# Kernel tuning notes

Hardware: AMD Instinct MI355X
Metric: run time of the kernel (lower is better)

## Reference

```python
import jax, jax.numpy as jnp
import numpy as np

TEMPERATURE = 0.4
N, D = 8192, 128

def _l2norm(x):
    return x / jnp.maximum(jnp.linalg.norm(x, axis=-1, keepdims=True), 1e-12)

def _semi_loss(z1, z2, temp):
    z1n = _l2norm(z1)
    z2n = _l2norm(z2)
    refl = jnp.exp(jnp.matmul(z1n, z1n.T) / temp)      # [N, N]
    between = jnp.exp(jnp.matmul(z1n, z2n.T) / temp)   # [N, N]
    pos = jnp.diagonal(between)
    denom = refl.sum(axis=1) + between.sum(axis=1) - jnp.diagonal(refl)
    return -jnp.log(pos / denom)

def setup_inputs() -> dict:
    key = jax.random.key(0)
    k1, k2 = jax.random.split(key)
    out = jax.random.normal(k1, (N, D), dtype=jnp.float32)
    aug_out = jax.random.normal(k2, (N, D), dtype=jnp.float32)
    return {"out": out, "aug_out": aug_out}

def reference(out, aug_out):
    l1 = _semi_loss(out, aug_out, TEMPERATURE)
    l2 = _semi_loss(aug_out, out, TEMPERATURE)
    loss = (l1 + l2) * 0.5
    return loss.mean()
```

## Files before the change

kernel.cpp:

```cpp
#include <hip/hip_runtime.h>
#include <hip/hip_bf16.h>

#define NR  8192
#define M   16384
#define SUBB 16384

constexpr float INV_T   = 2.5f;
constexpr float SCALE_S = 1.89914134f;
constexpr float E_REFL  = 12.182493960703473f;
constexpr unsigned UNIT_E8M0 = 0x7F7F7F7Fu;

typedef int   i32x4 __attribute__((ext_vector_type(4)));
typedef int   i32x8 __attribute__((ext_vector_type(8)));
typedef float f32x4 __attribute__((ext_vector_type(4)));

typedef const __attribute__((address_space(1))) unsigned int* gas_u32;
typedef __attribute__((address_space(3))) unsigned int*       las_u32;

__device__ __forceinline__ float fexp2(float x) {
#if __has_builtin(__builtin_amdgcn_exp2f)
    return __builtin_amdgcn_exp2f(x);
#else
    return exp2f(x);
#endif
}

__device__ __forceinline__ void stage_sub16(const char* __restrict__ gsrc,
                                            char* lds, int w, int lane) {
    #pragma unroll
    for (int it = 0; it < 4; ++it) {
        int off = w * 4096 + it * 1024 + lane * 16;
        int swz = off ^ (((off >> 7) & 7) << 4);
        __builtin_amdgcn_global_load_lds((gas_u32)(gsrc + swz),
                                         (las_u32)(lds + w * 4096 + it * 1024),
                                         16, 0, 0);
    }
}

__global__ __launch_bounds__(256) void norm_kernel(
    const float* __restrict__ outp, const float* __restrict__ augp,
    unsigned char* __restrict__ Zf8, float* __restrict__ R,
    float* __restrict__ posdot, float* __restrict__ outf)
{
    int gt = blockIdx.x * 256 + threadIdx.x;
    if (gt < M) R[gt] = 0.0f;
    if (gt == 0) outf[0] = 0.0f;

    const int w    = threadIdx.x >> 6;
    const int lane = threadIdx.x & 63;
    const int row  = blockIdx.x * 4 + w;

    float2 a = *(const float2*)(outp + row * 128 + lane * 2);
    float2 b = *(const float2*)(augp + row * 128 + lane * 2);

    float ssa = a.x * a.x + a.y * a.y;
    float ssb = b.x * b.x + b.y * b.y;
    #pragma unroll
    for (int m = 1; m < 64; m <<= 1) {
        ssa += __shfl_xor(ssa, m);
        ssb += __shfl_xor(ssb, m);
    }
    float inva = 1.0f / fmaxf(sqrtf(ssa), 1e-12f);
    float invb = 1.0f / fmaxf(sqrtf(ssb), 1e-12f);

    float xa0 = a.x * inva, xa1 = a.y * inva;
    float xb0 = b.x * invb, xb1 = b.y * invb;

    unsigned int pa = __builtin_amdgcn_cvt_pk_fp8_f32(xa0 * SCALE_S, xa1 * SCALE_S, 0, false);
    unsigned int pb = __builtin_amdgcn_cvt_pk_fp8_f32(xb0 * SCALE_S, xb1 * SCALE_S, 0, false);
    *(unsigned short*)(Zf8 + (size_t)row * 128 + lane * 2)        = (unsigned short)pa;
    *(unsigned short*)(Zf8 + (size_t)(NR + row) * 128 + lane * 2) = (unsigned short)pb;

    float d = xa0 * xb0 + xa1 * xb1;
    #pragma unroll
    for (int m = 1; m < 64; m <<= 1) d += __shfl_xor(d, m);
    if (lane == 0) posdot[row] = d;
}

__global__ __launch_bounds__(256, 4) void gram_kernel(
    const unsigned char* __restrict__ Zf8, float* __restrict__ R)
{
    __shared__ char buf[2][SUBB];

    const int tid  = threadIdx.x;
    const int w    = tid >> 6;
    const int lane = tid & 63;
    const int l16  = lane & 15;
    const int lg   = lane >> 4;
    const int ch   = blockIdx.x;
    const int rb   = blockIdx.y;

    const char* Zb = (const char*)Zf8;
    const char* Xg = Zb + (size_t)rb * 32768;
    const char* Yg = Zb + (size_t)ch * 65536;

    i32x8 afrag[4];
    #pragma unroll
    for (int rt = 0; rt < 4; ++rt)
        afrag[rt] = *(const i32x8*)(Xg + (w * 64 + rt * 16 + l16) * 128 + lg * 32);

    stage_sub16(Yg, buf[0], w, lane);
    __syncthreads();

    f32x4 rs[4];
    #pragma unroll
    for (int rt = 0; rt < 4; ++rt) rs[rt] = (f32x4){0.f, 0.f, 0.f, 0.f};
    const f32x4 zero4 = (f32x4){0.f, 0.f, 0.f, 0.f};

    const int key   = (l16 & 7) << 4;
    const int lbase = l16 * 128 + lg * 32;
    const int addrA = lbase ^ key;
    const int addrB = (lbase + 16) ^ key;

    #pragma unroll 1
    for (int s = 0; s < 4; ++s) {
        if (s + 1 < 4)
            stage_sub16(Yg + (size_t)(s + 1) * SUBB, buf[(s + 1) & 1], w, lane);

        const char* cur = buf[s & 1];

        #pragma unroll 1
        for (int cb = 0; cb < 2; ++cb) {
            #pragma unroll
            for (int ct = 0; ct < 4; ++ct) {
                const char* p = cur + (cb * 4 + ct) * 2048;
                i32x8 b8;
                *(i32x4*)&b8       = *(const i32x4*)(p + addrA);
                *((i32x4*)&b8 + 1) = *(const i32x4*)(p + addrB);
                #pragma unroll
                for (int rt = 0; rt < 4; ++rt) {
                    f32x4 d = __builtin_amdgcn_mfma_scale_f32_16x16x128_f8f6f4(
                        afrag[rt], b8, zero4,
                        0 , 0 ,
                        0, UNIT_E8M0, 0, UNIT_E8M0);
                    f32x4 e;
                    e[0] = fexp2(d[0]); e[1] = fexp2(d[1]);
                    e[2] = fexp2(d[2]); e[3] = fexp2(d[3]);
                    rs[rt] += e;
                }
            }
        }
        __syncthreads();
    }

    #pragma unroll
    for (int rt = 0; rt < 4; ++rt)
        #pragma unroll
        for (int q = 0; q < 4; ++q) {
            float v = rs[rt][q];
            v += __shfl_xor(v, 1);  v += __shfl_xor(v, 2);
            v += __shfl_xor(v, 4);  v += __shfl_xor(v, 8);
            if (l16 == 0)
                atomicAdd(&R[rb * 256 + w * 64 + rt * 16 + lg * 4 + q], v);
        }
}

__global__ __launch_bounds__(256) void final_kernel(
    const float* __restrict__ R, const float* __restrict__ posdot,
    float* __restrict__ outv)
{
    const int i = blockIdx.x * 256 + threadIdx.x;
    float d1 = R[i]      - E_REFL;
    float d2 = R[NR + i] - E_REFL;
    float local = -posdot[i] * INV_T + 0.5f * (logf(d1) + logf(d2));

    #pragma unroll
    for (int m = 1; m < 64; m <<= 1) local += __shfl_xor(local, m);
    if ((threadIdx.x & 63) == 0)
        atomicAdd(outv, local * (1.0f / NR));
}

extern "C" void kernel_launch(void* const* d_in, const int* in_sizes, int n_in,
                              void* d_out, int out_size, void* d_ws, size_t ws_size,
                              hipStream_t stream) {
    const float* outp = (const float*)d_in[0];
    const float* augp = (const float*)d_in[1];

    char* ws = (char*)d_ws;
    unsigned char* Zf8 = (unsigned char*)ws;
    float* R      = (float*)(ws + 2097152);
    float* posdot = (float*)(ws + 2097152 + 65536);
    float* outf   = (float*)d_out;

    hipLaunchKernelGGL(norm_kernel, dim3(2048), dim3(256), 0, stream,
                       outp, augp, Zf8, R, posdot, outf);

    hipLaunchKernelGGL(gram_kernel, dim3(32, 64), dim3(256), 0, stream,
                       Zf8, R);

    hipLaunchKernelGGL(final_kernel, dim3(32), dim3(256), 0, stream,
                       R, posdot, outf);
}
```

Before: 52.79 us.

## Exploit Gram matrix symmetry with triangular tiles and deterministic partial-sum reduction

```diff
diff --git a/kernel.cpp b/kernel.cpp
--- a/kernel.cpp
+++ b/kernel.cpp
@@ -3,7 +3,8 @@
 
 #define NR  8192
 #define M   16384
-#define SUBB 16384
+#define TB  32768
+#define NTILES 2080
 
 constexpr float INV_T   = 2.5f;
 constexpr float SCALE_S = 1.89914134f;
@@ -25,26 +26,12 @@
 #endif
 }
 
-__device__ __forceinline__ void stage_sub16(const char* __restrict__ gsrc,
-                                            char* lds, int w, int lane) {
-    #pragma unroll
-    for (int it = 0; it < 4; ++it) {
-        int off = w * 4096 + it * 1024 + lane * 16;
-        int swz = off ^ (((off >> 7) & 7) << 4);
-        __builtin_amdgcn_global_load_lds((gas_u32)(gsrc + swz),
-                                         (las_u32)(lds + w * 4096 + it * 1024),
-                                         16, 0, 0);
-    }
-}
-
 __global__ __launch_bounds__(256) void norm_kernel(
     const float* __restrict__ outp, const float* __restrict__ augp,
-    unsigned char* __restrict__ Zf8, float* __restrict__ R,
-    float* __restrict__ posdot, float* __restrict__ outf)
-{
-    int gt = blockIdx.x * 256 + threadIdx.x;
-    if (gt < M) R[gt] = 0.0f;
-    if (gt == 0) outf[0] = 0.0f;
+    unsigned char* __restrict__ Zf8, float* __restrict__ posdot,
+    float* __restrict__ outf)
+{
+    if (blockIdx.x == 0 && threadIdx.x == 0) outf[0] = 0.0f;
 
     const int w    = threadIdx.x >> 6;
     const int lane = threadIdx.x & 63;
@@ -78,28 +65,44 @@
 }
 
 __global__ __launch_bounds__(256, 4) void gram_kernel(
-    const unsigned char* __restrict__ Zf8, float* __restrict__ R)
-{
-    __shared__ char buf[2][SUBB];
+    const unsigned char* __restrict__ Zf8,
+    float* __restrict__ rowpart, float* __restrict__ colpart)
+{
+    __shared__ char  Ys[TB];
+    __shared__ float colLds[4][256];
+    __shared__ float rowLds[256];
 
     const int tid  = threadIdx.x;
     const int w    = tid >> 6;
     const int lane = tid & 63;
     const int l16  = lane & 15;
     const int lg   = lane >> 4;
-    const int ch   = blockIdx.x;
-    const int rb   = blockIdx.y;
+
+    const int bid = blockIdx.x;
+    int a = (int)((129.0f - sqrtf(16641.0f - 8.0f * (float)bid)) * 0.5f);
+    a = max(0, min(63, a));
+    while (64 * a - (a * (a - 1)) / 2 > bid) --a;
+    while (64 * (a + 1) - ((a + 1) * a) / 2 <= bid) ++a;
+    const int b = a + (bid - (64 * a - (a * (a - 1)) / 2));
 
     const char* Zb = (const char*)Zf8;
-    const char* Xg = Zb + (size_t)rb * 32768;
-    const char* Yg = Zb + (size_t)ch * 65536;
+    const char* Xg = Zb + (size_t)a * TB;
+    const char* Yg = Zb + (size_t)b * TB;
+
+    #pragma unroll
+    for (int it = 0; it < 8; ++it) {
+        int off = w * 8192 + it * 1024 + lane * 16;
+        int swz = off ^ (((off >> 7) & 7) << 4);
+        __builtin_amdgcn_global_load_lds((gas_u32)(Yg + swz),
+                                         (las_u32)(Ys + w * 8192 + it * 1024),
+                                         16, 0, 0);
+    }
 
     i32x8 afrag[4];
     #pragma unroll
     for (int rt = 0; rt < 4; ++rt)
         afrag[rt] = *(const i32x8*)(Xg + (w * 64 + rt * 16 + l16) * 128 + lg * 32);
 
-    stage_sub16(Yg, buf[0], w, lane);
     __syncthreads();
 
     f32x4 rs[4];
@@ -113,34 +116,31 @@
     const int addrB = (lbase + 16) ^ key;
 
     #pragma unroll 1
-    for (int s = 0; s < 4; ++s) {
-        if (s + 1 < 4)
-            stage_sub16(Yg + (size_t)(s + 1) * SUBB, buf[(s + 1) & 1], w, lane);
-
-        const char* cur = buf[s & 1];
-
-        #pragma unroll 1
-        for (int cb = 0; cb < 2; ++cb) {
+    for (int cb = 0; cb < 4; ++cb) {
+        #pragma unroll
+        for (int ct = 0; ct < 4; ++ct) {
+            const char* p = Ys + (cb * 4 + ct) * 2048;
+            i32x8 b8;
+            *(i32x4*)&b8       = *(const i32x4*)(p + addrA);
+            *((i32x4*)&b8 + 1) = *(const i32x4*)(p + addrB);
+
+            float cp = 0.0f;
             #pragma unroll
-            for (int ct = 0; ct < 4; ++ct) {
-                const char* p = cur + (cb * 4 + ct) * 2048;
-                i32x8 b8;
-                *(i32x4*)&b8       = *(const i32x4*)(p + addrA);
-                *((i32x4*)&b8 + 1) = *(const i32x4*)(p + addrB);
-                #pragma unroll
-                for (int rt = 0; rt < 4; ++rt) {
-                    f32x4 d = __builtin_amdgcn_mfma_scale_f32_16x16x128_f8f6f4(
-                        afrag[rt], b8, zero4,
-                        0 , 0 ,
-                        0, UNIT_E8M0, 0, UNIT_E8M0);
-                    f32x4 e;
-                    e[0] = fexp2(d[0]); e[1] = fexp2(d[1]);
-                    e[2] = fexp2(d[2]); e[3] = fexp2(d[3]);
-                    rs[rt] += e;
-                }
+            for (int rt = 0; rt < 4; ++rt) {
+                f32x4 d = __builtin_amdgcn_mfma_scale_f32_16x16x128_f8f6f4(
+                    afrag[rt], b8, zero4,
+                    0 , 0 ,
+                    0, UNIT_E8M0, 0, UNIT_E8M0);
+                f32x4 e;
+                e[0] = fexp2(d[0]); e[1] = fexp2(d[1]);
+                e[2] = fexp2(d[2]); e[3] = fexp2(d[3]);
+                rs[rt] += e;
+                cp += (e[0] + e[1]) + (e[2] + e[3]);
             }
+            cp += __shfl_xor(cp, 16);
+            cp += __shfl_xor(cp, 32);
+            if (lg == 0) colLds[w][(cb * 4 + ct) * 16 + l16] = cp;
         }
-        __syncthreads();
     }
 
     #pragma unroll
@@ -150,9 +150,33 @@
             float v = rs[rt][q];
             v += __shfl_xor(v, 1);  v += __shfl_xor(v, 2);
             v += __shfl_xor(v, 4);  v += __shfl_xor(v, 8);
-            if (l16 == 0)
-                atomicAdd(&R[rb * 256 + w * 64 + rt * 16 + lg * 4 + q], v);
+            if (l16 == 0) rowLds[w * 64 + rt * 16 + lg * 4 + q] = v;
         }
+    __syncthreads();
+
+    rowpart[bid * 256 + tid] = rowLds[tid];
+    if (a != b)
+        colpart[bid * 256 + tid] = colLds[0][tid] + colLds[1][tid]
+                                 + colLds[2][tid] + colLds[3][tid];
+}
+
+__global__ __launch_bounds__(256) void reduce_kernel(
+    const float* __restrict__ rowpart, const float* __restrict__ colpart,
+    float* __restrict__ R)
+{
+    const int r = blockIdx.x * 256 + threadIdx.x;
+    const int t = r >> 8;
+    const int i = r & 255;
+
+    float s = 0.0f;
+    const int St = 64 * t - (t * (t - 1)) / 2;
+    for (int bb = t; bb < 64; ++bb)
+        s += rowpart[(St + bb - t) * 256 + i];
+    for (int aa = 0; aa < t; ++aa) {
+        int bidA = 64 * aa - (aa * (aa - 1)) / 2 + (t - aa);
+        s += colpart[bidA * 256 + i];
+    }
+    R[r] = s;
 }
 
 __global__ __launch_bounds__(256) void final_kernel(
@@ -178,15 +202,20 @@
 
     char* ws = (char*)d_ws;
     unsigned char* Zf8 = (unsigned char*)ws;
-    float* R      = (float*)(ws + 2097152);
-    float* posdot = (float*)(ws + 2097152 + 65536);
-    float* outf   = (float*)d_out;
+    float* R       = (float*)(ws + 2097152);
+    float* posdot  = (float*)(ws + 2097152 + 65536);
+    float* rowpart = (float*)(ws + 2097152 + 65536 + 32768);
+    float* colpart = (float*)(ws + 2097152 + 65536 + 32768 + NTILES * 1024);
+    float* outf    = (float*)d_out;
 
     hipLaunchKernelGGL(norm_kernel, dim3(2048), dim3(256), 0, stream,
-                       outp, augp, Zf8, R, posdot, outf);
-
-    hipLaunchKernelGGL(gram_kernel, dim3(32, 64), dim3(256), 0, stream,
-                       Zf8, R);
+                       outp, augp, Zf8, posdot, outf);
+
+    hipLaunchKernelGGL(gram_kernel, dim3(NTILES), dim3(256), 0, stream,
+                       Zf8, rowpart, colpart);
+
+    hipLaunchKernelGGL(reduce_kernel, dim3(64), dim3(256), 0, stream,
+                       rowpart, colpart, R);
 
     hipLaunchKernelGGL(final_kernel, dim3(32), dim3(256), 0, stream,
                        R, posdot, outf);
```

Measured after the change: 62.28 us. 1.18x slower.
